# Kernel optimization log

Measured on AMD Instinct MI355X. Metric: run time of the kernel, lower is better.

## Reference

```python
import jax, jax.numpy as jnp
import numpy as np
from jax import lax

VOCAB = 50000
EMB = 10
HID = 16


def setup_inputs() -> dict:
    key = jax.random.key(0)
    ks = jax.random.split(key, 8)
    B, T = 4096, 512
    x = jax.random.randint(ks[0], (B, T), 0, VOCAB + 1)
    emb = jax.random.normal(ks[1], (VOCAB + 1, EMB), dtype=jnp.float32)
    emb = emb.at[0].set(0.0)  # padding_idx=0 row is zeros
    s_ih = 1.0 / np.sqrt(HID)
    Wih = jax.random.uniform(ks[2], (4 * HID, EMB), minval=-s_ih, maxval=s_ih, dtype=jnp.float32)
    Whh = jax.random.uniform(ks[3], (4 * HID, HID), minval=-s_ih, maxval=s_ih, dtype=jnp.float32)
    bih = jax.random.uniform(ks[4], (4 * HID,), minval=-s_ih, maxval=s_ih, dtype=jnp.float32)
    bhh = jax.random.uniform(ks[5], (4 * HID,), minval=-s_ih, maxval=s_ih, dtype=jnp.float32)
    Wfc = jax.random.uniform(ks[6], (1, HID), minval=-s_ih, maxval=s_ih, dtype=jnp.float32)
    bfc = jax.random.uniform(ks[7], (1,), minval=-s_ih, maxval=s_ih, dtype=jnp.float32)
    return {"x": x, "emb": emb, "Wih": Wih, "Whh": Whh, "bih": bih, "bhh": bhh, "Wfc": Wfc, "bfc": bfc}


def _lstm_last_h(xe, Wih, Whh, bih, bhh):
    # xe: [B, T, EMB] -> final hidden state [B, HID]. PyTorch gate order: i, f, g, o.
    B = xe.shape[0]
    h0 = jnp.zeros((B, HID), dtype=xe.dtype)
    c0 = jnp.zeros((B, HID), dtype=xe.dtype)
    # Precompute input projections for all timesteps: [T, B, 4H]
    xproj = jnp.einsum('btе,ge->btg'.replace('\u0435', 'e'), xe, Wih) + bih + bhh
    xproj = xproj.transpose(1, 0, 2)

    def step(carry, xp_t):
        h, c = carry
        gates = xp_t + h @ Whh.T  # [B, 4H]
        i, f, g, o = jnp.split(gates, 4, axis=-1)
        i = jax.nn.sigmoid(i)
        f = jax.nn.sigmoid(f)
        g = jnp.tanh(g)
        o = jax.nn.sigmoid(o)
        c = f * c + i * g
        h = o * jnp.tanh(c)
        return (h, c), None

    (h, _), _ = lax.scan(step, (h0, c0), xproj)
    return h


def reference(x, emb, Wih, Whh, bih, bhh, Wfc, bfc):
    xe = emb[x]  # [B, T, EMB] embedding lookup (padding row 0 is zero)
    h = _lstm_last_h(xe, Wih, Whh, bih, bhh)  # [B, HID]
    out = h @ Wfc.T + bfc  # [B, 1]
    return jax.nn.sigmoid(out)
```

## Files before the change

kernel.cpp:

```cpp
#include <hip/hip_runtime.h>

#define T_LEN 512
#define NHID 16
#define NEMB 10
#define VOCAB1 50001

typedef float v2f __attribute__((ext_vector_type(2)));

__global__ __launch_bounds__(256) void build_table(
    const float* __restrict__ emb, const float* __restrict__ Wih,
    const float* __restrict__ bih, const float* __restrict__ bhh,
    float* __restrict__ tbl)
{
    const int tid = blockIdx.x * 256 + threadIdx.x;
    if (tid >= VOCAB1 * 16) return;
    const int v = tid >> 4, j = tid & 15;
    float e[NEMB];
    #pragma unroll
    for (int i = 0; i < NEMB; ++i) e[i] = emb[v * NEMB + i];
    float o[4];
    #pragma unroll
    for (int q = 0; q < 4; ++q) {
        const int r = q * 16 + j;
        float a = bih[r] + bhh[r];
        #pragma unroll
        for (int i = 0; i < NEMB; ++i) a += e[i] * Wih[r * NEMB + i];
        o[q] = a;
    }
    ((float4*)tbl)[tid] = make_float4(o[0], o[1], o[2], o[3]);
}

__global__ __launch_bounds__(256) void lstm_tbl_kernel(
    const int*   __restrict__ x,
    const float* __restrict__ tbl,
    const float* __restrict__ Whh,
    const float* __restrict__ Wfc,
    const float* __restrict__ bfc,
    float*       __restrict__ out)
{
    __shared__ int   idx_lds[T_LEN][16];
    __shared__ float hx[4 * 64];

    const int tid  = threadIdx.x;
    const int wv   = tid >> 6;
    const int lane = tid & 63;
    const int j    = lane & 15;
    const int g    = lane >> 4;
    const int lb   = tid >> 4;
    const int batch = blockIdx.x * 16 + lb;

    for (int i = tid; i < 16 * T_LEN; i += 256) {
        int b = i >> 9;
        int t = i & (T_LEN - 1);
        idx_lds[t][b] = x[(blockIdx.x * 16 + b) * T_LEN + t];
    }

    v2f w[4][8];
    #pragma unroll
    for (int q = 0; q < 4; ++q) {
        const int r = j + 16 * q;
        #pragma unroll
        for (int p = 0; p < 8; ++p)
            w[q][p] = (v2f){Whh[r * NHID + 2 * p], Whh[r * NHID + 2 * p + 1]};
    }

    __syncthreads();

    v2f h2[8];
    #pragma unroll
    for (int p = 0; p < 8; ++p) h2[p] = (v2f){0.f, 0.f};
    float c = 0.f;

    const float NL2E  = -1.44269504088896f;
    const float NL2E2 = -2.88539008177793f;
    const int hxW = wv * 64;
    const float4* hp = (const float4*)&hx[hxW + g * 16];

    float4 tb = ((const float4*)tbl)[(long)idx_lds[0][lb] * 16 + j];
    int idx_n  = idx_lds[1][lb];

    #pragma unroll 2
    for (int t = 0; t < T_LEN; ++t) {
        float4 tbn;
        if (t + 1 < T_LEN)
            tbn = ((const float4*)tbl)[(long)idx_n * 16 + j];
        const int idx_nn = (t + 2 < T_LEN) ? idx_lds[t + 2][lb] : 0;

        v2f a0 = (v2f){tb.x, 0.f}, a1 = (v2f){tb.y, 0.f};
        v2f a2 = (v2f){tb.z, 0.f}, a3 = (v2f){tb.w, 0.f};
        #pragma unroll
        for (int p = 0; p < 8; ++p) {
            a0 += h2[p] * w[0][p];
            a1 += h2[p] * w[1][p];
            a2 += h2[p] * w[2][p];
            a3 += h2[p] * w[3][p];
        }
        const float vi = a0.x + a0.y, vf = a1.x + a1.y;
        const float vg = a2.x + a2.y, vo = a3.x + a3.y;

        const float ig = __builtin_amdgcn_rcpf(1.f + __builtin_amdgcn_exp2f(vi * NL2E));
        const float fg = __builtin_amdgcn_rcpf(1.f + __builtin_amdgcn_exp2f(vf * NL2E));
        const float gg = 2.f * __builtin_amdgcn_rcpf(1.f + __builtin_amdgcn_exp2f(vg * NL2E2)) - 1.f;
        const float og = __builtin_amdgcn_rcpf(1.f + __builtin_amdgcn_exp2f(vo * NL2E));

        c = fg * c + ig * gg;
        const float tc = 2.f * __builtin_amdgcn_rcpf(1.f + __builtin_amdgcn_exp2f(c * NL2E2)) - 1.f;
        const float hv = og * tc;

        hx[hxW + lane] = hv;
        const float4 b0 = hp[0], b1 = hp[1], b2 = hp[2], b3 = hp[3];
        h2[0] = (v2f){b0.x, b0.y}; h2[1] = (v2f){b0.z, b0.w};
        h2[2] = (v2f){b1.x, b1.y}; h2[3] = (v2f){b1.z, b1.w};
        h2[4] = (v2f){b2.x, b2.y}; h2[5] = (v2f){b2.z, b2.w};
        h2[6] = (v2f){b3.x, b3.y}; h2[7] = (v2f){b3.z, b3.w};

        tb = tbn; idx_n = idx_nn;
    }

    if (j == 0) {
        float logit = bfc[0];
        #pragma unroll
        for (int p = 0; p < 8; ++p)
            logit += h2[p].x * Wfc[2 * p] + h2[p].y * Wfc[2 * p + 1];
        out[batch] = __builtin_amdgcn_rcpf(1.f + __builtin_amdgcn_exp2f(logit * NL2E));
    }
}

__global__ __launch_bounds__(256) void lstm_fb_kernel(
    const int*   __restrict__ x,
    const float* __restrict__ emb,
    const float* __restrict__ Wih,
    const float* __restrict__ Whh,
    const float* __restrict__ bih,
    const float* __restrict__ bhh,
    const float* __restrict__ Wfc,
    const float* __restrict__ bfc,
    float*       __restrict__ out)
{
    __shared__ int   idx_lds[T_LEN][16];
    __shared__ float hx[4 * 64];

    const int tid  = threadIdx.x;
    const int wv   = tid >> 6;
    const int lane = tid & 63;
    const int j    = lane & 15;
    const int g    = lane >> 4;
    const int lb   = tid >> 4;
    const int batch = blockIdx.x * 16 + lb;

    for (int i = tid; i < 16 * T_LEN; i += 256) {
        int b = i >> 9;
        int t = i & (T_LEN - 1);
        idx_lds[t][b] = x[(blockIdx.x * 16 + b) * T_LEN + t];
    }

    float wih[4][NEMB], bias[4];
    v2f w[4][8];
    #pragma unroll
    for (int q = 0; q < 4; ++q) {
        const int r = j + 16 * q;
        #pragma unroll
        for (int e = 0; e < NEMB; ++e) wih[q][e] = Wih[r * NEMB + e];
        #pragma unroll
        for (int p = 0; p < 8; ++p)
            w[q][p] = (v2f){Whh[r * NHID + 2 * p], Whh[r * NHID + 2 * p + 1]};
        bias[q] = bih[r] + bhh[r];
    }

    __syncthreads();

    v2f h2[8];
    #pragma unroll
    for (int p = 0; p < 8; ++p) h2[p] = (v2f){0.f, 0.f};
    float c = 0.f;

    const float NL2E  = -1.44269504088896f;
    const float NL2E2 = -2.88539008177793f;
    const int hxW = wv * 64;
    const float4* hp = (const float4*)&hx[hxW + g * 16];

    float2 xa, xb, xc, xd, xe2;
    {
        const float2* er = (const float2*)(emb + (long)idx_lds[0][lb] * NEMB);
        xa = er[0]; xb = er[1]; xc = er[2]; xd = er[3]; xe2 = er[4];
    }
    int idx_n = idx_lds[1][lb];

    #pragma unroll 1
    for (int t = 0; t < T_LEN; ++t) {
        const float xv[NEMB] = {xa.x, xa.y, xb.x, xb.y, xc.x, xc.y,
                                xd.x, xd.y, xe2.x, xe2.y};
        if (t + 1 < T_LEN) {
            const float2* er = (const float2*)(emb + (long)idx_n * NEMB);
            xa = er[0]; xb = er[1]; xc = er[2]; xd = er[3]; xe2 = er[4];
        }
        const int idx_nn = (t + 2 < T_LEN) ? idx_lds[t + 2][lb] : 0;

        float v[4];
        #pragma unroll
        for (int q = 0; q < 4; ++q) {
            float a = bias[q];
            #pragma unroll
            for (int e = 0; e < NEMB; ++e) a += xv[e] * wih[q][e];
            v[q] = a;
        }
        v2f a0 = (v2f){v[0], 0.f}, a1 = (v2f){v[1], 0.f};
        v2f a2 = (v2f){v[2], 0.f}, a3 = (v2f){v[3], 0.f};
        #pragma unroll
        for (int p = 0; p < 8; ++p) {
            a0 += h2[p] * w[0][p];
            a1 += h2[p] * w[1][p];
            a2 += h2[p] * w[2][p];
            a3 += h2[p] * w[3][p];
        }
        const float vi = a0.x + a0.y, vf = a1.x + a1.y;
        const float vg = a2.x + a2.y, vo = a3.x + a3.y;

        const float ig = __builtin_amdgcn_rcpf(1.f + __builtin_amdgcn_exp2f(vi * NL2E));
        const float fg = __builtin_amdgcn_rcpf(1.f + __builtin_amdgcn_exp2f(vf * NL2E));
        const float gg = 2.f * __builtin_amdgcn_rcpf(1.f + __builtin_amdgcn_exp2f(vg * NL2E2)) - 1.f;
        const float og = __builtin_amdgcn_rcpf(1.f + __builtin_amdgcn_exp2f(vo * NL2E));

        c = fg * c + ig * gg;
        const float tc = 2.f * __builtin_amdgcn_rcpf(1.f + __builtin_amdgcn_exp2f(c * NL2E2)) - 1.f;
        const float hv = og * tc;

        hx[hxW + lane] = hv;
        const float4 b0 = hp[0], b1 = hp[1], b2 = hp[2], b3 = hp[3];
        h2[0] = (v2f){b0.x, b0.y}; h2[1] = (v2f){b0.z, b0.w};
        h2[2] = (v2f){b1.x, b1.y}; h2[3] = (v2f){b1.z, b1.w};
        h2[4] = (v2f){b2.x, b2.y}; h2[5] = (v2f){b2.z, b2.w};
        h2[6] = (v2f){b3.x, b3.y}; h2[7] = (v2f){b3.z, b3.w};

        idx_n = idx_nn;
    }

    if (j == 0) {
        float logit = bfc[0];
        #pragma unroll
        for (int p = 0; p < 8; ++p)
            logit += h2[p].x * Wfc[2 * p] + h2[p].y * Wfc[2 * p + 1];
        out[batch] = __builtin_amdgcn_rcpf(1.f + __builtin_amdgcn_exp2f(logit * NL2E));
    }
}

extern "C" void kernel_launch(void* const* d_in, const int* in_sizes, int n_in,
                              void* d_out, int out_size, void* d_ws, size_t ws_size,
                              hipStream_t stream) {
    const int*   x   = (const int*)  d_in[0];
    const float* emb = (const float*)d_in[1];
    const float* Wih = (const float*)d_in[2];
    const float* Whh = (const float*)d_in[3];
    const float* bih = (const float*)d_in[4];
    const float* bhh = (const float*)d_in[5];
    const float* Wfc = (const float*)d_in[6];
    const float* bfc = (const float*)d_in[7];
    float* outp = (float*)d_out;

    const int B = in_sizes[0] / T_LEN;
    const size_t TABLE_BYTES = (size_t)VOCAB1 * 64 * sizeof(float);

    if (ws_size >= TABLE_BYTES) {
        float* tbl = (float*)d_ws;
        build_table<<<(VOCAB1 * 16 + 255) / 256, 256, 0, stream>>>(emb, Wih, bih, bhh, tbl);
        lstm_tbl_kernel<<<B / 16, 256, 0, stream>>>(x, tbl, Whh, Wfc, bfc, outp);
    } else {
        lstm_fb_kernel<<<B / 16, 256, 0, stream>>>(x, emb, Wih, Whh, bih, bhh, Wfc, bfc, outp);
    }
}
```

Before: 173.8 us.

## Split each sequence across 32 lanes with two gates per lane

Measured after the change: 196.0 us. 12.8% more time.

```diff
diff --git a/kernel.cpp b/kernel.cpp
--- a/kernel.cpp
+++ b/kernel.cpp
@@ -27,10 +27,12 @@
         for (int i = 0; i < NEMB; ++i) a += e[i] * Wih[r * NEMB + i];
         o[q] = a;
     }
-    ((float4*)tbl)[tid] = make_float4(o[0], o[1], o[2], o[3]);
-}
-
-__global__ __launch_bounds__(256) void lstm_tbl_kernel(
+    float2* t2 = (float2*)tbl;
+    t2[v * 32 + j]      = make_float2(o[0], o[1]);
+    t2[v * 32 + 16 + j] = make_float2(o[2], o[3]);
+}
+
+__global__ __launch_bounds__(256) void lstm32_kernel(
     const int*   __restrict__ x,
     const float* __restrict__ tbl,
     const float* __restrict__ Whh,
@@ -38,30 +40,31 @@
     const float* __restrict__ bfc,
     float*       __restrict__ out)
 {
-    __shared__ int   idx_lds[T_LEN][16];
-    __shared__ float hx[4 * 64];
+    __shared__ int   idx_lds[T_LEN][8];
+    __shared__ float hx[8 * 16];
 
     const int tid  = threadIdx.x;
-    const int wv   = tid >> 6;
     const int lane = tid & 63;
     const int j    = lane & 15;
-    const int g    = lane >> 4;
-    const int lb   = tid >> 4;
-    const int batch = blockIdx.x * 16 + lb;
-
-    for (int i = tid; i < 16 * T_LEN; i += 256) {
+    const int hi   = (lane >> 4) & 1;
+    const int lb   = tid >> 5;
+    const int batch = blockIdx.x * 8 + lb;
+
+    for (int i = tid; i < 8 * T_LEN; i += 256) {
         int b = i >> 9;
         int t = i & (T_LEN - 1);
-        idx_lds[t][b] = x[(blockIdx.x * 16 + b) * T_LEN + t];
-    }
-
-    v2f w[4][8];
-    #pragma unroll
-    for (int q = 0; q < 4; ++q) {
-        const int r = j + 16 * q;
-        #pragma unroll
-        for (int p = 0; p < 8; ++p)
-            w[q][p] = (v2f){Whh[r * NHID + 2 * p], Whh[r * NHID + 2 * p + 1]};
+        idx_lds[t][b] = x[(blockIdx.x * 8 + b) * T_LEN + t];
+    }
+
+    v2f wA[8], wB[8];
+    {
+        const int rA = (2 * hi) * 16 + j;
+        const int rB = rA + 16;
+        #pragma unroll
+        for (int p = 0; p < 8; ++p) {
+            wA[p] = (v2f){Whh[rA * NHID + 2 * p], Whh[rA * NHID + 2 * p + 1]};
+            wB[p] = (v2f){Whh[rB * NHID + 2 * p], Whh[rB * NHID + 2 * p + 1]};
+        }
     }
 
     __syncthreads();
@@ -73,51 +76,59 @@
 
     const float NL2E  = -1.44269504088896f;
     const float NL2E2 = -2.88539008177793f;
-    const int hxW = wv * 64;
-    const float4* hp = (const float4*)&hx[hxW + g * 16];
-
-    float4 tb = ((const float4*)tbl)[(long)idx_lds[0][lb] * 16 + j];
-    int idx_n  = idx_lds[1][lb];
-
-    #pragma unroll 2
+    const bool  hib = (hi != 0);
+    const float sA = hib ? NL2E2 : NL2E;
+    const float mA = hib ? 2.f : 1.f;
+    const float bA = hib ? -1.f : 0.f;
+
+    const float2* tf2 = (const float2*)tbl;
+    const int foff = hi * 16 + j;
+    const float4* hp = (const float4*)&hx[lb * 16];
+
+    float2 tb0 = tf2[(long)idx_lds[0][lb] * 32 + foff];
+    float2 tb1 = tf2[(long)idx_lds[1][lb] * 32 + foff];
+    int    i2  = idx_lds[2][lb];
+
+    #pragma unroll 1
     for (int t = 0; t < T_LEN; ++t) {
-        float4 tbn;
-        if (t + 1 < T_LEN)
-            tbn = ((const float4*)tbl)[(long)idx_n * 16 + j];
-        const int idx_nn = (t + 2 < T_LEN) ? idx_lds[t + 2][lb] : 0;
-
-        v2f a0 = (v2f){tb.x, 0.f}, a1 = (v2f){tb.y, 0.f};
-        v2f a2 = (v2f){tb.z, 0.f}, a3 = (v2f){tb.w, 0.f};
+        float2 tb2 = make_float2(0.f, 0.f);
+        if (t + 2 < T_LEN) tb2 = tf2[(long)i2 * 32 + foff];
+        const int i3 = (t + 3 < T_LEN) ? idx_lds[t + 3][lb] : 0;
+
+        v2f aA = (v2f){tb0.x, 0.f}, aB = (v2f){tb0.y, 0.f};
         #pragma unroll
         for (int p = 0; p < 8; ++p) {
-            a0 += h2[p] * w[0][p];
-            a1 += h2[p] * w[1][p];
-            a2 += h2[p] * w[2][p];
-            a3 += h2[p] * w[3][p];
-        }
-        const float vi = a0.x + a0.y, vf = a1.x + a1.y;
-        const float vg = a2.x + a2.y, vo = a3.x + a3.y;
-
-        const float ig = __builtin_amdgcn_rcpf(1.f + __builtin_amdgcn_exp2f(vi * NL2E));
-        const float fg = __builtin_amdgcn_rcpf(1.f + __builtin_amdgcn_exp2f(vf * NL2E));
-        const float gg = 2.f * __builtin_amdgcn_rcpf(1.f + __builtin_amdgcn_exp2f(vg * NL2E2)) - 1.f;
-        const float og = __builtin_amdgcn_rcpf(1.f + __builtin_amdgcn_exp2f(vo * NL2E));
-
-        c = fg * c + ig * gg;
+            aA += h2[p] * wA[p];
+            aB += h2[p] * wB[p];
+        }
+        const float vA = aA.x + aA.y, vB = aB.x + aB.y;
+
+        const float gA = __builtin_amdgcn_rcpf(1.f + __builtin_amdgcn_exp2f(vA * sA)) * mA + bA;
+        const float gB = __builtin_amdgcn_rcpf(1.f + __builtin_amdgcn_exp2f(vB * NL2E));
+
+        const float othA = __shfl_xor(gA, 16, 64);
+        const float othB = __shfl_xor(gB, 16, 64);
+
+        const float ii = hib ? othA : gA;
+        const float ff = hib ? othB : gB;
+        const float gg = hib ? gA : othA;
+        const float oo = hib ? gB : othB;
+
+        c = ff * c + ii * gg;
         const float tc = 2.f * __builtin_amdgcn_rcpf(1.f + __builtin_amdgcn_exp2f(c * NL2E2)) - 1.f;
-        const float hv = og * tc;
-
-        hx[hxW + lane] = hv;
+        const float hv = oo * tc;
+
+        hx[lb * 16 + j] = hv;
         const float4 b0 = hp[0], b1 = hp[1], b2 = hp[2], b3 = hp[3];
         h2[0] = (v2f){b0.x, b0.y}; h2[1] = (v2f){b0.z, b0.w};
         h2[2] = (v2f){b1.x, b1.y}; h2[3] = (v2f){b1.z, b1.w};
         h2[4] = (v2f){b2.x, b2.y}; h2[5] = (v2f){b2.z, b2.w};
         h2[6] = (v2f){b3.x, b3.y}; h2[7] = (v2f){b3.z, b3.w};
 
-        tb = tbn; idx_n = idx_nn;
-    }
-
-    if (j == 0) {
+        tb0 = tb1; tb1 = tb2; i2 = i3;
+    }
+
+    if ((lane & 31) == 0) {
         float logit = bfc[0];
         #pragma unroll
         for (int p = 0; p < 8; ++p)
@@ -263,7 +274,7 @@
     if (ws_size >= TABLE_BYTES) {
         float* tbl = (float*)d_ws;
         build_table<<<(VOCAB1 * 16 + 255) / 256, 256, 0, stream>>>(emb, Wih, bih, bhh, tbl);
-        lstm_tbl_kernel<<<B / 16, 256, 0, stream>>>(x, tbl, Whh, Wfc, bfc, outp);
+        lstm32_kernel<<<B / 8, 256, 0, stream>>>(x, tbl, Whh, Wfc, bfc, outp);
     } else {
         lstm_fb_kernel<<<B / 16, 256, 0, stream>>>(x, emb, Wih, Whh, bih, bhh, Wfc, bfc, outp);
     }
```

## Interleave two batch sequences per thread and prefetch table rows deeper

Applied to the files above, without the earlier changes.

After: 340.5 us. 96.0% more time.

```diff
diff --git a/kernel.cpp b/kernel.cpp
--- a/kernel.cpp
+++ b/kernel.cpp
@@ -30,7 +30,7 @@
     ((float4*)tbl)[tid] = make_float4(o[0], o[1], o[2], o[3]);
 }
 
-__global__ __launch_bounds__(256) void lstm_tbl_kernel(
+__global__ __launch_bounds__(256) void lstm_ilp2_kernel(
     const int*   __restrict__ x,
     const float* __restrict__ tbl,
     const float* __restrict__ Whh,
@@ -38,22 +38,17 @@
     const float* __restrict__ bfc,
     float*       __restrict__ out)
 {
-    __shared__ int   idx_lds[T_LEN][16];
-    __shared__ float hx[4 * 64];
+    __shared__ float hx[32 * 16];
 
     const int tid  = threadIdx.x;
     const int wv   = tid >> 6;
     const int lane = tid & 63;
     const int j    = lane & 15;
     const int g    = lane >> 4;
-    const int lb   = tid >> 4;
-    const int batch = blockIdx.x * 16 + lb;
-
-    for (int i = tid; i < 16 * T_LEN; i += 256) {
-        int b = i >> 9;
-        int t = i & (T_LEN - 1);
-        idx_lds[t][b] = x[(blockIdx.x * 16 + b) * T_LEN + t];
-    }
+    const int lbA  = wv * 8 + g;
+    const int lbB  = lbA + 4;
+    const int bA   = blockIdx.x * 32 + lbA;
+    const int bB   = blockIdx.x * 32 + lbB;
 
     v2f w[4][8];
     #pragma unroll
@@ -64,28 +59,21 @@
             w[q][p] = (v2f){Whh[r * NHID + 2 * p], Whh[r * NHID + 2 * p + 1]};
     }
 
-    __syncthreads();
-
-    v2f h2[8];
-    #pragma unroll
-    for (int p = 0; p < 8; ++p) h2[p] = (v2f){0.f, 0.f};
-    float c = 0.f;
+    v2f hA[8], hB[8];
+    #pragma unroll
+    for (int p = 0; p < 8; ++p) { hA[p] = (v2f){0.f, 0.f}; hB[p] = (v2f){0.f, 0.f}; }
+    float cA = 0.f, cB = 0.f;
 
     const float NL2E  = -1.44269504088896f;
     const float NL2E2 = -2.88539008177793f;
-    const int hxW = wv * 64;
-    const float4* hp = (const float4*)&hx[hxW + g * 16];
-
-    float4 tb = ((const float4*)tbl)[(long)idx_lds[0][lb] * 16 + j];
-    int idx_n  = idx_lds[1][lb];
-
-    #pragma unroll 2
-    for (int t = 0; t < T_LEN; ++t) {
-        float4 tbn;
-        if (t + 1 < T_LEN)
-            tbn = ((const float4*)tbl)[(long)idx_n * 16 + j];
-        const int idx_nn = (t + 2 < T_LEN) ? idx_lds[t + 2][lb] : 0;
-
+
+    const float4* t4  = (const float4*)tbl;
+    const float4* hpA = (const float4*)&hx[lbA * 16];
+    const float4* hpB = (const float4*)&hx[lbB * 16];
+    const int* xA = x + (long)bA * T_LEN;
+    const int* xB = x + (long)bB * T_LEN;
+
+    auto step = [&](const float4& tb, v2f* h2, float& c) -> float {
         v2f a0 = (v2f){tb.x, 0.f}, a1 = (v2f){tb.y, 0.f};
         v2f a2 = (v2f){tb.z, 0.f}, a3 = (v2f){tb.w, 0.f};
         #pragma unroll
@@ -97,32 +85,58 @@
         }
         const float vi = a0.x + a0.y, vf = a1.x + a1.y;
         const float vg = a2.x + a2.y, vo = a3.x + a3.y;
-
         const float ig = __builtin_amdgcn_rcpf(1.f + __builtin_amdgcn_exp2f(vi * NL2E));
         const float fg = __builtin_amdgcn_rcpf(1.f + __builtin_amdgcn_exp2f(vf * NL2E));
         const float gg = 2.f * __builtin_amdgcn_rcpf(1.f + __builtin_amdgcn_exp2f(vg * NL2E2)) - 1.f;
         const float og = __builtin_amdgcn_rcpf(1.f + __builtin_amdgcn_exp2f(vo * NL2E));
-
         c = fg * c + ig * gg;
         const float tc = 2.f * __builtin_amdgcn_rcpf(1.f + __builtin_amdgcn_exp2f(c * NL2E2)) - 1.f;
-        const float hv = og * tc;
-
-        hx[hxW + lane] = hv;
-        const float4 b0 = hp[0], b1 = hp[1], b2 = hp[2], b3 = hp[3];
-        h2[0] = (v2f){b0.x, b0.y}; h2[1] = (v2f){b0.z, b0.w};
-        h2[2] = (v2f){b1.x, b1.y}; h2[3] = (v2f){b1.z, b1.w};
-        h2[4] = (v2f){b2.x, b2.y}; h2[5] = (v2f){b2.z, b2.w};
-        h2[6] = (v2f){b3.x, b3.y}; h2[7] = (v2f){b3.z, b3.w};
-
-        tb = tbn; idx_n = idx_nn;
+        return og * tc;
+    };
+
+    float4 tA0 = t4[(long)xA[0] * 16 + j];
+    float4 tB0 = t4[(long)xB[0] * 16 + j];
+    float4 tA1 = t4[(long)xA[1] * 16 + j];
+    float4 tB1 = t4[(long)xB[1] * 16 + j];
+    int iA2 = xA[2], iB2 = xB[2];
+
+    #pragma unroll 1
+    for (int t = 0; t < T_LEN; ++t) {
+        const float4 tA2 = t4[(long)iA2 * 16 + j];
+        const float4 tB2 = t4[(long)iB2 * 16 + j];
+        const int iA3 = (t + 3 < T_LEN) ? xA[t + 3] : 0;
+        const int iB3 = (t + 3 < T_LEN) ? xB[t + 3] : 0;
+
+        const float hvA = step(tA0, hA, cA);
+        hx[lbA * 16 + j] = hvA;
+
+        const float hvB = step(tB0, hB, cB);
+        hx[lbB * 16 + j] = hvB;
+
+        const float4 a0 = hpA[0], a1 = hpA[1], a2 = hpA[2], a3 = hpA[3];
+        const float4 b0 = hpB[0], b1 = hpB[1], b2 = hpB[2], b3 = hpB[3];
+        hA[0] = (v2f){a0.x, a0.y}; hA[1] = (v2f){a0.z, a0.w};
+        hA[2] = (v2f){a1.x, a1.y}; hA[3] = (v2f){a1.z, a1.w};
+        hA[4] = (v2f){a2.x, a2.y}; hA[5] = (v2f){a2.z, a2.w};
+        hA[6] = (v2f){a3.x, a3.y}; hA[7] = (v2f){a3.z, a3.w};
+        hB[0] = (v2f){b0.x, b0.y}; hB[1] = (v2f){b0.z, b0.w};
+        hB[2] = (v2f){b1.x, b1.y}; hB[3] = (v2f){b1.z, b1.w};
+        hB[4] = (v2f){b2.x, b2.y}; hB[5] = (v2f){b2.z, b2.w};
+        hB[6] = (v2f){b3.x, b3.y}; hB[7] = (v2f){b3.z, b3.w};
+
+        tA0 = tA1; tA1 = tA2; iA2 = iA3;
+        tB0 = tB1; tB1 = tB2; iB2 = iB3;
     }
 
     if (j == 0) {
-        float logit = bfc[0];
-        #pragma unroll
-        for (int p = 0; p < 8; ++p)
-            logit += h2[p].x * Wfc[2 * p] + h2[p].y * Wfc[2 * p + 1];
-        out[batch] = __builtin_amdgcn_rcpf(1.f + __builtin_amdgcn_exp2f(logit * NL2E));
+        float lgA = bfc[0], lgB = bfc[0];
+        #pragma unroll
+        for (int p = 0; p < 8; ++p) {
+            lgA += hA[p].x * Wfc[2 * p] + hA[p].y * Wfc[2 * p + 1];
+            lgB += hB[p].x * Wfc[2 * p] + hB[p].y * Wfc[2 * p + 1];
+        }
+        out[bA] = __builtin_amdgcn_rcpf(1.f + __builtin_amdgcn_exp2f(lgA * NL2E));
+        out[bB] = __builtin_amdgcn_rcpf(1.f + __builtin_amdgcn_exp2f(lgB * NL2E));
     }
 }
 
@@ -263,7 +277,7 @@
     if (ws_size >= TABLE_BYTES) {
         float* tbl = (float*)d_ws;
         build_table<<<(VOCAB1 * 16 + 255) / 256, 256, 0, stream>>>(emb, Wih, bih, bhh, tbl);
-        lstm_tbl_kernel<<<B / 16, 256, 0, stream>>>(x, tbl, Whh, Wfc, bfc, outp);
+        lstm_ilp2_kernel<<<B / 32, 256, 0, stream>>>(x, tbl, Whh, Wfc, bfc, outp);
     } else {
         lstm_fb_kernel<<<B / 16, 256, 0, stream>>>(x, emb, Wih, Whh, bih, bhh, Wfc, bfc, outp);
     }
```
